# Optimization experiments

Measured on AMD Instinct MI355X. Metric: run time of the kernel, lower is better.

## Reference

```python
import jax, jax.numpy as jnp
import numpy as np

NUM_HEADS = 16


def setup_inputs() -> dict:
    key = jax.random.key(0)
    ks = jax.random.split(key, 8)
    B, S, D = 2, 2048, 1024
    q = jax.random.normal(ks[0], (B, S, D), dtype=jnp.float32)
    k = jax.random.normal(ks[1], (B, S, D), dtype=jnp.float32)
    v = jax.random.normal(ks[2], (B, S, D), dtype=jnp.float32)
    mask = jax.random.randint(ks[3], (1, 1, S, S), 0, 2, dtype=jnp.int32)
    sc = 1.0 / np.sqrt(D)
    wq = jax.random.normal(ks[4], (D, D), dtype=jnp.float32) * sc
    wk = jax.random.normal(ks[5], (D, D), dtype=jnp.float32) * sc
    wv = jax.random.normal(ks[6], (D, D), dtype=jnp.float32) * sc
    wout = jax.random.normal(ks[7], (D, D), dtype=jnp.float32) * sc
    return {"q": q, "k": k, "v": v, "mask": mask,
            "wq": wq, "wk": wk, "wv": wv, "wout": wout}


def reference(q, k, v, mask, wq, wk, wv, wout):
    B, S, D = q.shape
    H = NUM_HEADS
    hd = D // H

    def proj(x, w):
        # nn.Linear(bias=False): x @ w.T, then split heads -> [B,H,S,hd]
        return (x @ w.T).reshape(B, -1, H, hd).transpose(0, 2, 1, 3)

    qh, kh, vh = proj(q, wq), proj(k, wk), proj(v, wv)
    scale = jnp.asarray(hd, q.dtype) ** 0.5
    scores = jnp.einsum('bhqd,bhkd->bhqk', qh, kh) / scale  # [B,H,S,S]
    att = jax.nn.softmax(scores, axis=-1)
    # NOTE: original applies masked_fill AFTER softmax with value -1e-9
    att = jnp.where(mask == 0, jnp.asarray(-1e-9, att.dtype), att)
    out = jnp.einsum('bhqk,bhkd->bhqd', att, vh)  # [B,H,S,hd]
    out = out.transpose(0, 2, 1, 3).reshape(B, S, D)
    return out @ wout.T
```

## Files before the change

### kernel.cpp

```cpp
#include <hip/hip_runtime.h>
#include <stdint.h>


#define BATCH  2
#define S_LEN  2048
#define DMODEL 1024
#define NH     16
#define HD     64

typedef __bf16 bf16_t;
typedef short  short8 __attribute__((ext_vector_type(8)));
typedef float  f32x4  __attribute__((ext_vector_type(4)));

#define AS1 __attribute__((address_space(1)))
#define AS3 __attribute__((address_space(3)))

static constexpr size_t MB = (size_t)1 << 20;
static constexpr size_t WS_REQUIRED = 112 * MB;
#define OFF_XHI(z)  ((size_t)(z) * 16 * MB)
#define OFF_XLO(z)  (OFF_XHI(z) + 8 * MB)
#define OFF_WHI(z)  (48 * MB + (size_t)(z) * 4 * MB)
#define OFF_WLO(z)  (OFF_WHI(z) + 2 * MB)
#define OFF_PHI(z)  (64 * MB + (size_t)(z) * 16 * MB)
#define OFF_PLO(z)  (OFF_PHI(z) + 8 * MB)
#define OFF_OHI     ((size_t)0)
#define OFF_OLO     (8 * MB)
#define OFF_MASKB   (16 * MB)

__device__ __forceinline__ f32x4 mfma_bf16(short8 a, short8 b, f32x4 c) {
    return __builtin_amdgcn_mfma_f32_16x16x32_bf16(a, b, c, 0, 0, 0);
}

__device__ __forceinline__ short8 ld8(const bf16_t* p) {
    return *reinterpret_cast<const short8*>(p);
}

__global__ void cvt_split_kernel(const float* __restrict__ x,
                                 bf16_t* __restrict__ hi, bf16_t* __restrict__ lo,
                                 int n) {
    int i = (blockIdx.x * blockDim.x + threadIdx.x) * 4;
    if (i >= n) return;
    const float4 v = *reinterpret_cast<const float4*>(x + i);
    float s[4] = {v.x, v.y, v.z, v.w};
    ushort hbits[4], lbits[4];
#pragma unroll
    for (int j = 0; j < 4; j++) {
        bf16_t hh = (bf16_t)s[j];
        bf16_t ll = (bf16_t)(s[j] - (float)hh);
        hbits[j] = __builtin_bit_cast(ushort, hh);
        lbits[j] = __builtin_bit_cast(ushort, ll);
    }
    *reinterpret_cast<ushort4*>(hi + i) = ushort4{hbits[0], hbits[1], hbits[2], hbits[3]};
    *reinterpret_cast<ushort4*>(lo + i) = ushort4{lbits[0], lbits[1], lbits[2], lbits[3]};
}

__global__ void cvt_mask_kernel(const int* __restrict__ m, bf16_t* __restrict__ mb, int n) {
    int i = (blockIdx.x * blockDim.x + threadIdx.x) * 4;
    if (i >= n) return;
    const int4 v = *reinterpret_cast<const int4*>(m + i);
    int s[4] = {v.x, v.y, v.z, v.w};
    ushort b[4];
#pragma unroll
    for (int j = 0; j < 4; j++) {
        bf16_t t = (bf16_t)(s[j] ? 1.0f : 0.0f);
        b[j] = __builtin_bit_cast(ushort, t);
    }
    *reinterpret_cast<ushort4*>(mb + i) = ushort4{b[0], b[1], b[2], b[3]};
}

template <int FINAL>
__global__ __launch_bounds__(256, 2) void gemm_split_kernel(char* __restrict__ ws,
                                                            float* __restrict__ fout) {
    __shared__ __align__(16) bf16_t AsH[128 * 32];
    __shared__ __align__(16) bf16_t AsL[128 * 32];
    __shared__ __align__(16) bf16_t BsH[128 * 32];
    __shared__ __align__(16) bf16_t BsL[128 * 32];

    const int z = FINAL ? 3 : blockIdx.z;
    const bf16_t* Ahi = FINAL ? (const bf16_t*)(ws + OFF_OHI) : (const bf16_t*)(ws + OFF_XHI(z));
    const bf16_t* Alo = FINAL ? (const bf16_t*)(ws + OFF_OLO) : (const bf16_t*)(ws + OFF_XLO(z));
    const bf16_t* Bhi = (const bf16_t*)(ws + OFF_WHI(z));
    const bf16_t* Blo = (const bf16_t*)(ws + OFF_WLO(z));
    bf16_t* Ohi = FINAL ? nullptr : (bf16_t*)(ws + OFF_PHI(z));
    bf16_t* Olo = FINAL ? nullptr : (bf16_t*)(ws + OFF_PLO(z));
    const float scale = (!FINAL && z == 0) ? 0.18033688011112042f : 1.0f;

    const int tid = threadIdx.x;
    const int lane = tid & 63, w = tid >> 6;
    const int wr = w >> 1, wc = w & 1;
    const int fr = lane & 15, fg = lane >> 4;
    const int m0 = blockIdx.x * 128, n0 = blockIdx.y * 128;
    const int K = 1024;

    f32x4 acc[4][4];
#pragma unroll
    for (int i = 0; i < 4; i++)
#pragma unroll
        for (int j = 0; j < 4; j++) acc[i][j] = f32x4{0.f, 0.f, 0.f, 0.f};

    AS3 bf16_t* asAH = (AS3 bf16_t*)AsH;
    AS3 bf16_t* asAL = (AS3 bf16_t*)AsL;
    AS3 bf16_t* asBH = (AS3 bf16_t*)BsH;
    AS3 bf16_t* asBL = (AS3 bf16_t*)BsL;

#pragma unroll 1
    for (int ks = 0; ks < K; ks += 32) {
        __syncthreads();
#pragma unroll
        for (int i = 0; i < 2; i++) {
            const int c = i * 256 + tid;
            const int row = c >> 2;
            const int ce = (c & 3) * 8;
            const size_t gA = (size_t)(m0 + row) * K + ks + ce;
            const size_t gB = (size_t)(n0 + row) * K + ks + ce;
            const size_t d = (size_t)(i * 256 + w * 64) * 8;
            __builtin_amdgcn_global_load_lds((const AS1 void*)(Ahi + gA), (AS3 void*)(asAH + d), 16, 0, 0);
            __builtin_amdgcn_global_load_lds((const AS1 void*)(Alo + gA), (AS3 void*)(asAL + d), 16, 0, 0);
            __builtin_amdgcn_global_load_lds((const AS1 void*)(Bhi + gB), (AS3 void*)(asBH + d), 16, 0, 0);
            __builtin_amdgcn_global_load_lds((const AS1 void*)(Blo + gB), (AS3 void*)(asBL + d), 16, 0, 0);
        }
        __syncthreads();

        short8 afh[4], afl[4], bfh[4], bfl[4];
#pragma unroll
        for (int i = 0; i < 4; i++) {
            const int ao = (wr * 64 + i * 16 + fr) * 32 + fg * 8;
            const int bo = (wc * 64 + i * 16 + fr) * 32 + fg * 8;
            afh[i] = ld8(&AsH[ao]);
            afl[i] = ld8(&AsL[ao]);
            bfh[i] = ld8(&BsH[bo]);
            bfl[i] = ld8(&BsL[bo]);
        }
#pragma unroll
        for (int i = 0; i < 4; i++)
#pragma unroll
            for (int j = 0; j < 4; j++) {
                acc[i][j] = mfma_bf16(afh[i], bfh[j], acc[i][j]);
                acc[i][j] = mfma_bf16(afh[i], bfl[j], acc[i][j]);
                acc[i][j] = mfma_bf16(afl[i], bfh[j], acc[i][j]);
            }
    }

#pragma unroll
    for (int i = 0; i < 4; i++) {
#pragma unroll
        for (int j = 0; j < 4; j++) {
            const int ncol = n0 + wc * 64 + j * 16 + fr;
#pragma unroll
            for (int r = 0; r < 4; r++) {
                const int m = m0 + wr * 64 + i * 16 + fg * 4 + r;
                const float val = acc[i][j][r] * scale;
                if (FINAL) {
                    fout[(size_t)m * DMODEL + ncol] = val;
                } else {
                    const bf16_t h = (bf16_t)val;
                    const bf16_t l = (bf16_t)(val - (float)h);
                    const int b = m >> 11, s = m & (S_LEN - 1);
                    const int hh = ncol >> 6, d = ncol & (HD - 1);
                    size_t idx;
                    if (z == 2) idx = ((size_t)(b * NH + hh) * HD + d) * S_LEN + s;
                    else        idx = ((size_t)(b * NH + hh) * S_LEN + s) * HD + d;
                    Ohi[idx] = h;
                    Olo[idx] = l;
                }
            }
        }
    }
}

__global__ __launch_bounds__(256, 2) void attn_kernel(char* __restrict__ ws) {
    __shared__ __align__(16) bf16_t KsH[2][8 * 64 * 8];
    __shared__ __align__(16) bf16_t KsL[2][8 * 64 * 8];
    __shared__ __align__(16) bf16_t VsH[8 * 64 * 8];
    __shared__ __align__(16) bf16_t VsL[8 * 64 * 8];

    const bf16_t* Qhi = (const bf16_t*)(ws + OFF_PHI(0));
    const bf16_t* Qlo = (const bf16_t*)(ws + OFF_PLO(0));
    const bf16_t* Khi = (const bf16_t*)(ws + OFF_PHI(1));
    const bf16_t* Klo = (const bf16_t*)(ws + OFF_PLO(1));
    const bf16_t* Vhi = (const bf16_t*)(ws + OFF_PHI(2));
    const bf16_t* Vlo = (const bf16_t*)(ws + OFF_PLO(2));
    const bf16_t* Mb  = (const bf16_t*)(ws + OFF_MASKB);
    bf16_t* Ohi = (bf16_t*)(ws + OFF_OHI);
    bf16_t* Olo = (bf16_t*)(ws + OFF_OLO);

    const int tid = threadIdx.x, lane = tid & 63, w = tid >> 6;
    const int fr = lane & 15, fg = lane >> 4;
    const int bh = blockIdx.y;
    const int q0 = blockIdx.x * 64;
    const int qrow = q0 + w * 16 + fr;
    const size_t qkBase = (size_t)bh * S_LEN * HD;
    const size_t vtBase = (size_t)bh * HD * S_LEN;

    size_t kSrc[2], vSrc[2];
#pragma unroll
    for (int i = 0; i < 2; i++) {
        const int s = i * 256 + tid;
        const int l = s & 63, f = (s >> 6) & 7;
        const int sfr = l & 15, sfg = l >> 4;
        const int cf = f >> 1, kc = f & 1;
        const int r = (cf & 1) * 4 + (sfr & 3) + (sfr >> 2) * 8 + (cf >> 1) * 32;
        kSrc[i] = qkBase + (size_t)r * HD + kc * 32 + sfg * 8;
        vSrc[i] = vtBase + (size_t)((f >> 1) * 16 + sfr) * S_LEN + (f & 1) * 32 + sfg * 8;
    }

    short8 qh[2], ql[2];
#pragma unroll
    for (int kc = 0; kc < 2; kc++) {
        const size_t off = qkBase + (size_t)qrow * HD + kc * 32 + fg * 8;
        qh[kc] = ld8(Qhi + off);
        ql[kc] = ld8(Qlo + off);
    }

    f32x4 acco[4];
#pragma unroll
    for (int df = 0; df < 4; df++) acco[df] = f32x4{0.f, 0.f, 0.f, 0.f};
    float mrun = -__builtin_inff(), lrun = 0.f;

    const size_t mrowBase = (size_t)qrow * S_LEN;

#define STAGE_K(K0, BUF)                                                                           \
    {                                                                                              \
        _Pragma("unroll") for (int i = 0; i < 2; i++) {                                            \
            const size_t ko = kSrc[i] + (size_t)(K0) * HD;                                         \
            const size_t dst = (size_t)(i * 256 + w * 64) * 8;                                     \
            __builtin_amdgcn_global_load_lds((const AS1 void*)(Khi + ko),                          \
                                             (AS3 void*)((AS3 bf16_t*)KsH[BUF] + dst), 16, 0, 0);  \
            __builtin_amdgcn_global_load_lds((const AS1 void*)(Klo + ko),                          \
                                             (AS3 void*)((AS3 bf16_t*)KsL[BUF] + dst), 16, 0, 0);  \
        }                                                                                          \
    }
#define STAGE_V(K0)                                                                                \
    {                                                                                              \
        _Pragma("unroll") for (int i = 0; i < 2; i++) {                                            \
            const size_t vo = vSrc[i] + (K0);                                                      \
            const size_t dst = (size_t)(i * 256 + w * 64) * 8;                                     \
            __builtin_amdgcn_global_load_lds((const AS1 void*)(Vhi + vo),                          \
                                             (AS3 void*)((AS3 bf16_t*)VsH + dst), 16, 0, 0);       \
            __builtin_amdgcn_global_load_lds((const AS1 void*)(Vlo + vo),                          \
                                             (AS3 void*)((AS3 bf16_t*)VsL + dst), 16, 0, 0);       \
        }                                                                                          \
    }

    STAGE_K(0, 0)
    short8 mv0Cur = ld8(Mb + mrowBase + fg * 8);
    short8 mv1Cur = ld8(Mb + mrowBase + 32 + fg * 8);
    short8 mv0Nxt = mv0Cur, mv1Nxt = mv1Cur;
    __syncthreads();

    int cur = 0;
#pragma unroll 1
    for (int k0 = 0; k0 < S_LEN; k0 += 64) {
        STAGE_V(k0)
        if (k0 + 64 < S_LEN) {
            STAGE_K(k0 + 64, cur ^ 1)
            mv0Nxt = ld8(Mb + mrowBase + (k0 + 64) + fg * 8);
            mv1Nxt = ld8(Mb + mrowBase + (k0 + 64) + 32 + fg * 8);
        }

        f32x4 sacc[4];
#pragma unroll
        for (int cf = 0; cf < 4; cf++) sacc[cf] = f32x4{0.f, 0.f, 0.f, 0.f};
        __builtin_amdgcn_s_setprio(1);
#pragma unroll
        for (int cf = 0; cf < 4; cf++) {
#pragma unroll
            for (int kc = 0; kc < 2; kc++) {
                const int fi = cf * 2 + kc;
                const short8 kh = ld8(&KsH[cur][(fi * 64 + lane) * 8]);
                const short8 kl = ld8(&KsL[cur][(fi * 64 + lane) * 8]);
                sacc[cf] = mfma_bf16(kh, qh[kc], sacc[cf]);
                sacc[cf] = mfma_bf16(kl, qh[kc], sacc[cf]);
                sacc[cf] = mfma_bf16(kh, ql[kc], sacc[cf]);
            }
        }
        __builtin_amdgcn_s_setprio(0);

        float mx = sacc[0][0];
#pragma unroll
        for (int cf = 0; cf < 4; cf++)
#pragma unroll
            for (int r = 0; r < 4; r++) mx = fmaxf(mx, sacc[cf][r]);
        mx = fmaxf(mx, __shfl_xor(mx, 16, 64));
        mx = fmaxf(mx, __shfl_xor(mx, 32, 64));
        if (!__all(mx <= mrun + 8.0f)) {
            const float mnew = fmaxf(mrun, mx);
            const float alpha = exp2f(mrun - mnew);
            mrun = mnew;
            lrun *= alpha;
#pragma unroll
            for (int df = 0; df < 4; df++) acco[df] *= alpha;
        }

        float p[4][4], psum = 0.f;
#pragma unroll
        for (int cf = 0; cf < 4; cf++)
#pragma unroll
            for (int r = 0; r < 4; r++) {
                p[cf][r] = exp2f(sacc[cf][r] - mrun);
                psum += p[cf][r];
            }
        psum += __shfl_xor(psum, 16, 64);
        psum += __shfl_xor(psum, 32, 64);
        lrun += psum;

        short8 phi[2], plo[2];
#pragma unroll
        for (int kc2 = 0; kc2 < 2; kc2++) {
#pragma unroll
            for (int j = 0; j < 8; j++) {
                const int cf = kc2 * 2 + (j >> 2), r = j & 3;
                const float mvf = (float)__builtin_bit_cast(
                    bf16_t, (ushort)((cf >> 1) ? mv1Cur[(cf & 1) * 4 + r] : mv0Cur[(cf & 1) * 4 + r]));
                const float pm = p[cf][r] * mvf;
                const bf16_t h = (bf16_t)pm;
                const bf16_t l = (bf16_t)(pm - (float)h);
                phi[kc2][j] = __builtin_bit_cast(short, h);
                plo[kc2][j] = __builtin_bit_cast(short, l);
            }
        }

        __syncthreads();

        __builtin_amdgcn_s_setprio(1);
#pragma unroll
        for (int kc2 = 0; kc2 < 2; kc2++) {
#pragma unroll
            for (int df = 0; df < 4; df++) {
                const int fi = df * 2 + kc2;
                const short8 vh = ld8(&VsH[(fi * 64 + lane) * 8]);
                const short8 vl = ld8(&VsL[(fi * 64 + lane) * 8]);
                acco[df] = mfma_bf16(vh, phi[kc2], acco[df]);
                acco[df] = mfma_bf16(vl, phi[kc2], acco[df]);
                acco[df] = mfma_bf16(vh, plo[kc2], acco[df]);
            }
        }
        __builtin_amdgcn_s_setprio(0);

        __syncthreads();
        mv0Cur = mv0Nxt;
        mv1Cur = mv1Nxt;
        cur ^= 1;
    }
#undef STAGE_K
#undef STAGE_V

    const int b = bh >> 4, hh = bh & (NH - 1);
    const float inv = 1.0f / lrun;
    const size_t obase = ((size_t)b * S_LEN + qrow) * DMODEL + hh * HD;
#pragma unroll
    for (int df = 0; df < 4; df++) {
#pragma unroll
        for (int r = 0; r < 4; r++) {
            const int d = df * 16 + fg * 4 + r;
            const float o = acco[df][r] * inv;
            const bf16_t h = (bf16_t)o;
            Ohi[obase + d] = h;
            Olo[obase + d] = (bf16_t)(o - (float)h);
        }
    }
}

extern "C" void kernel_launch(void* const* d_in, const int* in_sizes, int n_in,
                              void* d_out, int out_size, void* d_ws, size_t ws_size,
                              hipStream_t stream) {
    (void)in_sizes; (void)n_in; (void)out_size;
    if (ws_size < WS_REQUIRED) return;

    const float* q    = (const float*)d_in[0];
    const float* k    = (const float*)d_in[1];
    const float* v    = (const float*)d_in[2];
    const int*   mask = (const int*)  d_in[3];
    const float* wq   = (const float*)d_in[4];
    const float* wk   = (const float*)d_in[5];
    const float* wv   = (const float*)d_in[6];
    const float* wout = (const float*)d_in[7];
    char* ws = (char*)d_ws;
    float* out = (float*)d_out;

    const size_t nX = (size_t)BATCH * S_LEN * DMODEL;
    const size_t nW = (size_t)DMODEL * DMODEL;
    const size_t nM = (size_t)S_LEN * S_LEN;
    const dim3 blk(256);

    cvt_split_kernel<<<dim3(nX / 1024), blk, 0, stream>>>(q, (bf16_t*)(ws + OFF_XHI(0)), (bf16_t*)(ws + OFF_XLO(0)), (int)nX);
    cvt_split_kernel<<<dim3(nX / 1024), blk, 0, stream>>>(k, (bf16_t*)(ws + OFF_XHI(1)), (bf16_t*)(ws + OFF_XLO(1)), (int)nX);
    cvt_split_kernel<<<dim3(nX / 1024), blk, 0, stream>>>(v, (bf16_t*)(ws + OFF_XHI(2)), (bf16_t*)(ws + OFF_XLO(2)), (int)nX);
    cvt_split_kernel<<<dim3(nW / 1024), blk, 0, stream>>>(wq,   (bf16_t*)(ws + OFF_WHI(0)), (bf16_t*)(ws + OFF_WLO(0)), (int)nW);
    cvt_split_kernel<<<dim3(nW / 1024), blk, 0, stream>>>(wk,   (bf16_t*)(ws + OFF_WHI(1)), (bf16_t*)(ws + OFF_WLO(1)), (int)nW);
    cvt_split_kernel<<<dim3(nW / 1024), blk, 0, stream>>>(wv,   (bf16_t*)(ws + OFF_WHI(2)), (bf16_t*)(ws + OFF_WLO(2)), (int)nW);
    cvt_split_kernel<<<dim3(nW / 1024), blk, 0, stream>>>(wout, (bf16_t*)(ws + OFF_WHI(3)), (bf16_t*)(ws + OFF_WLO(3)), (int)nW);

    gemm_split_kernel<0><<<dim3(32, 8, 3), blk, 0, stream>>>(ws, nullptr);

    cvt_mask_kernel<<<dim3(nM / 1024), blk, 0, stream>>>(mask, (bf16_t*)(ws + OFF_MASKB), (int)nM);

    attn_kernel<<<dim3(S_LEN / 64, BATCH * NH), blk, 0, stream>>>(ws);

    gemm_split_kernel<1><<<dim3(32, 8, 1), blk, 0, stream>>>(ws, out);
}
```

Before: 438.1 us.

## Process two query fragments per wave in attention kernel to reuse K/V tiles

Each wave now handles 32 query rows (two 16-row MFMA fragments) instead of 16, so a block covers 128 queries and the grid halves. Every K and V fragment read from LDS feeds twice as many MFMAs, and the K/V global-to-LDS staging is shared by more queries, cutting memory traffic per query. The cost is doubled accumulator, score and mask registers, which may lower occupancy, and only 512 blocks remain to fill the GPU.

```diff
diff --git a/kernel.cpp b/kernel.cpp
--- a/kernel.cpp
+++ b/kernel.cpp
@@ -187,8 +187,8 @@
     const int tid = threadIdx.x, lane = tid & 63, w = tid >> 6;
     const int fr = lane & 15, fg = lane >> 4;
     const int bh = blockIdx.y;
-    const int q0 = blockIdx.x * 64;
-    const int qrow = q0 + w * 16 + fr;
+    const int q0 = blockIdx.x * 128;
+    const int qrow0 = q0 + w * 32 + fr;
     const size_t qkBase = (size_t)bh * S_LEN * HD;
     const size_t vtBase = (size_t)bh * HD * S_LEN;
 
@@ -204,20 +204,26 @@
         vSrc[i] = vtBase + (size_t)((f >> 1) * 16 + sfr) * S_LEN + (f & 1) * 32 + sfg * 8;
     }
 
-    short8 qh[2], ql[2];
-#pragma unroll
-    for (int kc = 0; kc < 2; kc++) {
-        const size_t off = qkBase + (size_t)qrow * HD + kc * 32 + fg * 8;
-        qh[kc] = ld8(Qhi + off);
-        ql[kc] = ld8(Qlo + off);
-    }
-
-    f32x4 acco[4];
-#pragma unroll
-    for (int df = 0; df < 4; df++) acco[df] = f32x4{0.f, 0.f, 0.f, 0.f};
-    float mrun = -__builtin_inff(), lrun = 0.f;
-
-    const size_t mrowBase = (size_t)qrow * S_LEN;
+    short8 qh[2][2], ql[2][2];
+#pragma unroll
+    for (int mf = 0; mf < 2; mf++)
+#pragma unroll
+        for (int kc = 0; kc < 2; kc++) {
+            const size_t off = qkBase + (size_t)(qrow0 + mf * 16) * HD + kc * 32 + fg * 8;
+            qh[mf][kc] = ld8(Qhi + off);
+            ql[mf][kc] = ld8(Qlo + off);
+        }
+
+    f32x4 acco[2][4];
+#pragma unroll
+    for (int mf = 0; mf < 2; mf++)
+#pragma unroll
+        for (int df = 0; df < 4; df++) acco[mf][df] = f32x4{0.f, 0.f, 0.f, 0.f};
+    float mrun[2] = {-__builtin_inff(), -__builtin_inff()};
+    float lrun[2] = {0.f, 0.f};
+
+    const size_t mrowBase0 = (size_t)qrow0 * S_LEN;
+    const size_t mrowBase1 = (size_t)(qrow0 + 16) * S_LEN;
 
 #define STAGE_K(K0, BUF)                                                                           \
     {                                                                                              \
@@ -243,9 +249,15 @@
     }
 
     STAGE_K(0, 0)
-    short8 mv0Cur = ld8(Mb + mrowBase + fg * 8);
-    short8 mv1Cur = ld8(Mb + mrowBase + 32 + fg * 8);
-    short8 mv0Nxt = mv0Cur, mv1Nxt = mv1Cur;
+    short8 mvCur[2][2], mvNxt[2][2];
+    mvCur[0][0] = ld8(Mb + mrowBase0 + fg * 8);
+    mvCur[0][1] = ld8(Mb + mrowBase0 + 32 + fg * 8);
+    mvCur[1][0] = ld8(Mb + mrowBase1 + fg * 8);
+    mvCur[1][1] = ld8(Mb + mrowBase1 + 32 + fg * 8);
+#pragma unroll
+    for (int mf = 0; mf < 2; mf++)
+#pragma unroll
+        for (int hh = 0; hh < 2; hh++) mvNxt[mf][hh] = mvCur[mf][hh];
     __syncthreads();
 
     int cur = 0;
@@ -254,13 +266,17 @@
         STAGE_V(k0)
         if (k0 + 64 < S_LEN) {
             STAGE_K(k0 + 64, cur ^ 1)
-            mv0Nxt = ld8(Mb + mrowBase + (k0 + 64) + fg * 8);
-            mv1Nxt = ld8(Mb + mrowBase + (k0 + 64) + 32 + fg * 8);
-        }
-
-        f32x4 sacc[4];
-#pragma unroll
-        for (int cf = 0; cf < 4; cf++) sacc[cf] = f32x4{0.f, 0.f, 0.f, 0.f};
+            mvNxt[0][0] = ld8(Mb + mrowBase0 + (k0 + 64) + fg * 8);
+            mvNxt[0][1] = ld8(Mb + mrowBase0 + (k0 + 64) + 32 + fg * 8);
+            mvNxt[1][0] = ld8(Mb + mrowBase1 + (k0 + 64) + fg * 8);
+            mvNxt[1][1] = ld8(Mb + mrowBase1 + (k0 + 64) + 32 + fg * 8);
+        }
+
+        f32x4 sacc[2][4];
+#pragma unroll
+        for (int mf = 0; mf < 2; mf++)
+#pragma unroll
+            for (int cf = 0; cf < 4; cf++) sacc[mf][cf] = f32x4{0.f, 0.f, 0.f, 0.f};
         __builtin_amdgcn_s_setprio(1);
 #pragma unroll
         for (int cf = 0; cf < 4; cf++) {
@@ -269,56 +285,63 @@
                 const int fi = cf * 2 + kc;
                 const short8 kh = ld8(&KsH[cur][(fi * 64 + lane) * 8]);
                 const short8 kl = ld8(&KsL[cur][(fi * 64 + lane) * 8]);
-                sacc[cf] = mfma_bf16(kh, qh[kc], sacc[cf]);
-                sacc[cf] = mfma_bf16(kl, qh[kc], sacc[cf]);
-                sacc[cf] = mfma_bf16(kh, ql[kc], sacc[cf]);
+#pragma unroll
+                for (int mf = 0; mf < 2; mf++) {
+                    sacc[mf][cf] = mfma_bf16(kh, qh[mf][kc], sacc[mf][cf]);
+                    sacc[mf][cf] = mfma_bf16(kl, qh[mf][kc], sacc[mf][cf]);
+                    sacc[mf][cf] = mfma_bf16(kh, ql[mf][kc], sacc[mf][cf]);
+                }
             }
         }
         __builtin_amdgcn_s_setprio(0);
 
-        float mx = sacc[0][0];
-#pragma unroll
-        for (int cf = 0; cf < 4; cf++)
-#pragma unroll
-            for (int r = 0; r < 4; r++) mx = fmaxf(mx, sacc[cf][r]);
-        mx = fmaxf(mx, __shfl_xor(mx, 16, 64));
-        mx = fmaxf(mx, __shfl_xor(mx, 32, 64));
-        if (!__all(mx <= mrun + 8.0f)) {
-            const float mnew = fmaxf(mrun, mx);
-            const float alpha = exp2f(mrun - mnew);
-            mrun = mnew;
-            lrun *= alpha;
-#pragma unroll
-            for (int df = 0; df < 4; df++) acco[df] *= alpha;
-        }
-
-        float p[4][4], psum = 0.f;
-#pragma unroll
-        for (int cf = 0; cf < 4; cf++)
-#pragma unroll
-            for (int r = 0; r < 4; r++) {
-                p[cf][r] = exp2f(sacc[cf][r] - mrun);
-                psum += p[cf][r];
-            }
-        psum += __shfl_xor(psum, 16, 64);
-        psum += __shfl_xor(psum, 32, 64);
-        lrun += psum;
-
-        short8 phi[2], plo[2];
-#pragma unroll
-        for (int kc2 = 0; kc2 < 2; kc2++) {
-#pragma unroll
-            for (int j = 0; j < 8; j++) {
-                const int cf = kc2 * 2 + (j >> 2), r = j & 3;
-                const float mvf = (float)__builtin_bit_cast(
-                    bf16_t, (ushort)((cf >> 1) ? mv1Cur[(cf & 1) * 4 + r] : mv0Cur[(cf & 1) * 4 + r]));
-                const float pm = p[cf][r] * mvf;
-                const bf16_t h = (bf16_t)pm;
-                const bf16_t l = (bf16_t)(pm - (float)h);
-                phi[kc2][j] = __builtin_bit_cast(short, h);
-                plo[kc2][j] = __builtin_bit_cast(short, l);
-            }
-        }
+        float p[2][4][4];
+#pragma unroll
+        for (int mf = 0; mf < 2; mf++) {
+            float mx = sacc[mf][0][0];
+#pragma unroll
+            for (int cf = 0; cf < 4; cf++)
+#pragma unroll
+                for (int r = 0; r < 4; r++) mx = fmaxf(mx, sacc[mf][cf][r]);
+            mx = fmaxf(mx, __shfl_xor(mx, 16, 64));
+            mx = fmaxf(mx, __shfl_xor(mx, 32, 64));
+            if (!__all(mx <= mrun[mf] + 8.0f)) {
+                const float mnew = fmaxf(mrun[mf], mx);
+                const float alpha = exp2f(mrun[mf] - mnew);
+                mrun[mf] = mnew;
+                lrun[mf] *= alpha;
+#pragma unroll
+                for (int df = 0; df < 4; df++) acco[mf][df] *= alpha;
+            }
+            float psum = 0.f;
+#pragma unroll
+            for (int cf = 0; cf < 4; cf++)
+#pragma unroll
+                for (int r = 0; r < 4; r++) {
+                    p[mf][cf][r] = exp2f(sacc[mf][cf][r] - mrun[mf]);
+                    psum += p[mf][cf][r];
+                }
+            psum += __shfl_xor(psum, 16, 64);
+            psum += __shfl_xor(psum, 32, 64);
+            lrun[mf] += psum;
+        }
+
+        short8 phi[2][2], plo[2][2];
+#pragma unroll
+        for (int mf = 0; mf < 2; mf++)
+#pragma unroll
+            for (int kc2 = 0; kc2 < 2; kc2++)
+#pragma unroll
+                for (int j = 0; j < 8; j++) {
+                    const int cf = kc2 * 2 + (j >> 2), r = j & 3;
+                    const float mvf = (float)__builtin_bit_cast(
+                        bf16_t, (ushort)(mvCur[mf][cf >> 1][(cf & 1) * 4 + r]));
+                    const float pm = p[mf][cf][r] * mvf;
+                    const bf16_t h = (bf16_t)pm;
+                    const bf16_t l = (bf16_t)(pm - (float)h);
+                    phi[mf][kc2][j] = __builtin_bit_cast(short, h);
+                    plo[mf][kc2][j] = __builtin_bit_cast(short, l);
+                }
 
         __syncthreads();
 
@@ -330,33 +353,41 @@
                 const int fi = df * 2 + kc2;
                 const short8 vh = ld8(&VsH[(fi * 64 + lane) * 8]);
                 const short8 vl = ld8(&VsL[(fi * 64 + lane) * 8]);
-                acco[df] = mfma_bf16(vh, phi[kc2], acco[df]);
-                acco[df] = mfma_bf16(vl, phi[kc2], acco[df]);
-                acco[df] = mfma_bf16(vh, plo[kc2], acco[df]);
+#pragma unroll
+                for (int mf = 0; mf < 2; mf++) {
+                    acco[mf][df] = mfma_bf16(vh, phi[mf][kc2], acco[mf][df]);
+                    acco[mf][df] = mfma_bf16(vl, phi[mf][kc2], acco[mf][df]);
+                    acco[mf][df] = mfma_bf16(vh, plo[mf][kc2], acco[mf][df]);
+                }
             }
         }
         __builtin_amdgcn_s_setprio(0);
 
         __syncthreads();
-        mv0Cur = mv0Nxt;
-        mv1Cur = mv1Nxt;
+#pragma unroll
+        for (int mf = 0; mf < 2; mf++)
+#pragma unroll
+            for (int hh = 0; hh < 2; hh++) mvCur[mf][hh] = mvNxt[mf][hh];
         cur ^= 1;
     }
 #undef STAGE_K
 #undef STAGE_V
 
     const int b = bh >> 4, hh = bh & (NH - 1);
-    const float inv = 1.0f / lrun;
-    const size_t obase = ((size_t)b * S_LEN + qrow) * DMODEL + hh * HD;
-#pragma unroll
-    for (int df = 0; df < 4; df++) {
-#pragma unroll
-        for (int r = 0; r < 4; r++) {
-            const int d = df * 16 + fg * 4 + r;
-            const float o = acco[df][r] * inv;
-            const bf16_t h = (bf16_t)o;
-            Ohi[obase + d] = h;
-            Olo[obase + d] = (bf16_t)(o - (float)h);
+#pragma unroll
+    for (int mf = 0; mf < 2; mf++) {
+        const float inv = 1.0f / lrun[mf];
+        const size_t obase = ((size_t)b * S_LEN + qrow0 + mf * 16) * DMODEL + hh * HD;
+#pragma unroll
+        for (int df = 0; df < 4; df++) {
+#pragma unroll
+            for (int r = 0; r < 4; r++) {
+                const int d = df * 16 + fg * 4 + r;
+                const float o = acco[mf][df][r] * inv;
+                const bf16_t h = (bf16_t)o;
+                Ohi[obase + d] = h;
+                Olo[obase + d] = (bf16_t)(o - (float)h);
+            }
         }
     }
 }
@@ -395,7 +426,7 @@
 
     cvt_mask_kernel<<<dim3(nM / 1024), blk, 0, stream>>>(mask, (bf16_t*)(ws + OFF_MASKB), (int)nM);
 
-    attn_kernel<<<dim3(S_LEN / 64, BATCH * NH), blk, 0, stream>>>(ws);
+    attn_kernel<<<dim3(S_LEN / 128, BATCH * NH), blk, 0, stream>>>(ws);
 
     gemm_split_kernel<1><<<dim3(32, 8, 1), blk, 0, stream>>>(ws, out);
 }
```

After: 419.3 us. -4.3%, faster.
